# Kernel tuning notes

Hardware: AMD Instinct MI355X
Metric: run time of the kernel (lower is better)

Reference implementation:

```python
import jax, jax.numpy as jnp
import numpy as np

CYCLE_LEN = 168
CHANNEL_SIZE = 64
BATCH = 2048

def setup_inputs() -> dict:
    key = jax.random.key(0)
    k1, k2 = jax.random.split(key)
    index = jax.random.randint(k1, (BATCH,), 0, CYCLE_LEN, dtype=jnp.int64 if jax.config.jax_enable_x64 else jnp.int32)
    data = jax.random.normal(k2, (CYCLE_LEN, CHANNEL_SIZE), dtype=jnp.float32) * 0.1
    return {"index": index, "length": 720, "data": data}

def reference(index, length, data):
    # out[b, t, :] = data[(index[b] + t) % cycle_len]
    cycle_len = data.shape[0]
    gather_idx = (index[:, None] + jnp.arange(length)) % cycle_len  # [B, L]
    return data[gather_idx]  # [B, L, C]
```

## Files before the change

kernel.cpp:

```cpp
#include <hip/hip_runtime.h>


using f4 = __attribute__((ext_vector_type(4))) float;

constexpr int CCH   = 64;
constexpr int C4    = CCH / 4;
constexpr int BLOCK = 256;

__global__ __launch_bounds__(BLOCK) void recurrent_cycle_kernel(
    const int* __restrict__ index,
    const f4*  __restrict__ data4,
    f4*        __restrict__ out4,
    int L, int cycle_len)
{
    const int tid = threadIdx.x;
    const int b   = blockIdx.x;

    const int idx = index[b];
    f4* outb = out4 + (size_t)b * (size_t)L * C4;
    const int n = L * C4;

    const int t0 = tid >> 4;
    const int c4 = tid & (C4 - 1);
    int row = (idx + t0) % cycle_len;
    const int rstep = (BLOCK / C4) % cycle_len;

    #pragma unroll 3
    for (int p = tid; p < n; p += BLOCK) {
        f4 v = data4[row * C4 + c4];
        __builtin_nontemporal_store(v, &outb[p]);
        row += rstep;
        if (row >= cycle_len) row -= cycle_len;
    }
}

extern "C" void kernel_launch(void* const* d_in, const int* in_sizes, int n_in,
                              void* d_out, int out_size, void* d_ws, size_t ws_size,
                              hipStream_t stream) {
    const int*   index = (const int*)d_in[0];
    const float* data  = (const float*)d_in[2];

    const int B         = in_sizes[0];
    const int cycle_len = in_sizes[2] / CCH;
    const int L         = out_size / (B * CCH);

    recurrent_cycle_kernel<<<B, BLOCK, 0, stream>>>(
        index, (const f4*)data, (f4*)d_out, L, cycle_len);
}
```

Measured before the change: 79.99 us.

## Add specialized kernel preloading the cycle's rows into registers

Adds a templated fast path for cycle length 168 and L=720. Each thread loads the 21 distinct rows it will ever write into registers once, then emits a fully unrolled run of 45 stores. This removes repeated global loads and the per-iteration modulo bookkeeping. It also swaps nontemporal stores for plain stores and adds register pressure from the 21 f4 values.

Result: faster. 76.09 us (-4.9%).

```diff
diff --git a/kernel.cpp b/kernel.cpp
--- a/kernel.cpp
+++ b/kernel.cpp
@@ -6,8 +6,41 @@
 constexpr int CCH   = 64;
 constexpr int C4    = CCH / 4;
 constexpr int BLOCK = 256;
+constexpr int CYC   = 168;
+constexpr int RSTEP = BLOCK / C4;
+constexpr int NR    = 21;
 
-__global__ __launch_bounds__(BLOCK) void recurrent_cycle_kernel(
+template <int ITERS>
+__global__ __launch_bounds__(BLOCK) void rc_fast(
+    const int* __restrict__ index,
+    const f4*  __restrict__ data4,
+    f4*        __restrict__ out4,
+    int L)
+{
+    const int tid = threadIdx.x;
+    const int b   = blockIdx.x;
+
+    const int t0 = tid >> 4;
+    const int c4 = tid & (C4 - 1);
+    const int r0 = (index[b] + t0) % CYC;
+
+    f4 v[NR];
+    #pragma unroll
+    for (int j = 0; j < NR; ++j) {
+        int row = r0 + RSTEP * j;
+        if (row >= 2 * CYC) row -= 2 * CYC;
+        else if (row >= CYC) row -= CYC;
+        v[j] = data4[row * C4 + c4];
+    }
+
+    f4* outb = out4 + (size_t)b * (size_t)L * C4 + tid;
+    #pragma unroll
+    for (int p = 0; p < ITERS; ++p) {
+        outb[p * BLOCK] = v[p % NR];
+    }
+}
+
+__global__ __launch_bounds__(BLOCK) void rc_generic(
     const int* __restrict__ index,
     const f4*  __restrict__ data4,
     f4*        __restrict__ out4,
@@ -15,20 +48,15 @@
 {
     const int tid = threadIdx.x;
     const int b   = blockIdx.x;
-
     const int idx = index[b];
     f4* outb = out4 + (size_t)b * (size_t)L * C4;
-    const int n = L * C4;
-
+    const int n  = L * C4;
     const int t0 = tid >> 4;
     const int c4 = tid & (C4 - 1);
     int row = (idx + t0) % cycle_len;
-    const int rstep = (BLOCK / C4) % cycle_len;
-
-    #pragma unroll 3
+    const int rstep = RSTEP % cycle_len;
     for (int p = tid; p < n; p += BLOCK) {
-        f4 v = data4[row * C4 + c4];
-        __builtin_nontemporal_store(v, &outb[p]);
+        outb[p] = data4[row * C4 + c4];
         row += rstep;
         if (row >= cycle_len) row -= cycle_len;
     }
@@ -44,6 +72,11 @@
     const int cycle_len = in_sizes[2] / CCH;
     const int L         = out_size / (B * CCH);
 
-    recurrent_cycle_kernel<<<B, BLOCK, 0, stream>>>(
-        index, (const f4*)data, (f4*)d_out, L, cycle_len);
+    if (cycle_len == CYC && L == 720) {
+        rc_fast<720 * C4 / BLOCK><<<B, BLOCK, 0, stream>>>(
+            index, (const f4*)data, (f4*)d_out, L);
+    } else {
+        rc_generic<<<B, BLOCK, 0, stream>>>(
+            index, (const f4*)data, (f4*)d_out, L, cycle_len);
+    }
 }
```

## Add shape-specialized grid-stride kernel with compile-time constants and plain stores

Applied to the files above, without the earlier changes.

Adds a templated kernel specialized for B=2048, L=720, cycle_len=168. It uses a fixed 1024-block grid-stride loop over the flattened output, with the divide and modulo done on compile-time constants. Nontemporal stores become regular stores in both paths. The aim is to cut per-block launch and tail overhead and to make the address math cheaper. The cost is a per-element index load and division, plus a dependence on one hardcoded shape; other shapes fall back to the generic kernel.

Result: faster. 67.06 us (-16.2%).

```diff
diff --git a/kernel.cpp b/kernel.cpp
--- a/kernel.cpp
+++ b/kernel.cpp
@@ -6,8 +6,28 @@
 constexpr int CCH   = 64;
 constexpr int C4    = CCH / 4;
 constexpr int BLOCK = 256;
+constexpr unsigned GRIDB = 1024;
 
-__global__ __launch_bounds__(BLOCK) void recurrent_cycle_kernel(
+template <unsigned ROWF4, unsigned CYC, unsigned ITERS>
+__global__ __launch_bounds__(BLOCK) void rc_stride(
+    const int* __restrict__ index,
+    const f4*  __restrict__ data4,
+    f4*        __restrict__ out4)
+{
+    const unsigned G = GRIDB * BLOCK;
+    unsigned p = blockIdx.x * BLOCK + threadIdx.x;
+    #pragma unroll 4
+    for (unsigned i = 0; i < ITERS; ++i, p += G) {
+        unsigned b   = p / ROWF4;
+        unsigned q   = p - b * ROWF4;
+        unsigned t   = q >> 4;
+        unsigned c4  = q & (C4 - 1);
+        unsigned row = ((unsigned)index[b] + t) % CYC;
+        out4[p] = data4[row * C4 + c4];
+    }
+}
+
+__global__ __launch_bounds__(BLOCK) void rc_generic(
     const int* __restrict__ index,
     const f4*  __restrict__ data4,
     f4*        __restrict__ out4,
@@ -15,20 +35,15 @@
 {
     const int tid = threadIdx.x;
     const int b   = blockIdx.x;
-
     const int idx = index[b];
     f4* outb = out4 + (size_t)b * (size_t)L * C4;
-    const int n = L * C4;
-
+    const int n  = L * C4;
     const int t0 = tid >> 4;
     const int c4 = tid & (C4 - 1);
     int row = (idx + t0) % cycle_len;
     const int rstep = (BLOCK / C4) % cycle_len;
-
-    #pragma unroll 3
     for (int p = tid; p < n; p += BLOCK) {
-        f4 v = data4[row * C4 + c4];
-        __builtin_nontemporal_store(v, &outb[p]);
+        outb[p] = data4[row * C4 + c4];
         row += rstep;
         if (row >= cycle_len) row -= cycle_len;
     }
@@ -44,6 +59,11 @@
     const int cycle_len = in_sizes[2] / CCH;
     const int L         = out_size / (B * CCH);
 
-    recurrent_cycle_kernel<<<B, BLOCK, 0, stream>>>(
-        index, (const f4*)data, (f4*)d_out, L, cycle_len);
+    if (B == 2048 && L == 720 && cycle_len == 168) {
+        rc_stride<720 * C4, 168, 90><<<GRIDB, BLOCK, 0, stream>>>(
+            index, (const f4*)data, (f4*)d_out);
+    } else {
+        rc_generic<<<B, BLOCK, 0, stream>>>(
+            index, (const f4*)data, (f4*)d_out, L, cycle_len);
+    }
 }
```
